# Performance work log

Hardware: AMD Instinct MI355X
Metric: run time of the kernel (lower is better)

Reference implementation:

```python
import jax, jax.numpy as jnp
import numpy as np

NEG_SLOPE = 0.2  # PyG GATConv default
EPS = 1e-5       # BatchNorm1d default


def gat_conv(x, src, dst, W, a_src, a_dst, b, concat, num_nodes):
    # x: [N, Fin], W: [Fin, H*C], a_src/a_dst: [H, C], b: [H*C] or [C]
    H, C = a_src.shape
    h = (x @ W).reshape(num_nodes, H, C)           # [N, H, C]
    e_src = (h * a_src).sum(-1)                    # [N, H]
    e_dst = (h * a_dst).sum(-1)                    # [N, H]
    e = jax.nn.leaky_relu(e_src[src] + e_dst[dst], NEG_SLOPE)  # [E, H]
    # softmax over incoming edges per destination node (stable)
    m = jax.ops.segment_max(e, dst, num_segments=num_nodes)    # [N, H]
    ee = jnp.exp(e - m[dst])
    denom = jax.ops.segment_sum(ee, dst, num_segments=num_nodes)
    alpha = ee / denom[dst]                        # [E, H]
    out = jax.ops.segment_sum(alpha[:, :, None] * h[src], dst,
                              num_segments=num_nodes)          # [N, H, C]
    out = out.reshape(num_nodes, H * C) if concat else out.mean(axis=1)
    return out + b


def batchnorm(x, gamma, beta):
    mu = x.mean(axis=0)
    var = x.var(axis=0)
    return (x - mu) * jax.lax.rsqrt(var + EPS) * gamma + beta


def setup_inputs() -> dict:
    key = jax.random.key(0)
    ks = jax.random.split(key, 16)
    N, E, Fin, Hd, H, L = 50000, 800000, 256, 64, 4, 64
    s = 0.05
    inp = {
        "x": jax.random.normal(ks[0], (N, Fin), jnp.float32),
        "edge_index": jax.random.randint(ks[1], (2, E), 0, N, jnp.int64),
        # GAT layer 1 (concat=True -> out dim H*Hd = 256)
        "W1": jax.random.normal(ks[2], (Fin, H * Hd), jnp.float32) * s,
        "a_src1": jax.random.normal(ks[3], (H, Hd), jnp.float32) * s,
        "a_dst1": jax.random.normal(ks[4], (H, Hd), jnp.float32) * s,
        "b1": jnp.zeros((H * Hd,), jnp.float32),
        "gamma1": jnp.ones((H * Hd,), jnp.float32),
        "beta1": jnp.zeros((H * Hd,), jnp.float32),
        # conv_mean (concat=False -> out dim L)
        "Wm": jax.random.normal(ks[5], (H * Hd, H * L), jnp.float32) * s,
        "am_src": jax.random.normal(ks[6], (H, L), jnp.float32) * s,
        "am_dst": jax.random.normal(ks[7], (H, L), jnp.float32) * s,
        "bm": jnp.zeros((L,), jnp.float32),
        # conv_log_std
        "Ws": jax.random.normal(ks[8], (H * Hd, H * L), jnp.float32) * s,
        "as_src": jax.random.normal(ks[9], (H, L), jnp.float32) * s,
        "as_dst": jax.random.normal(ks[10], (H, L), jnp.float32) * s,
        "bs": jnp.zeros((L,), jnp.float32),
    }
    return inp


def reference(x, edge_index, W1, a_src1, a_dst1, b1, gamma1, beta1,
              Wm, am_src, am_dst, bm, Ws, as_src, as_dst, bs):
    N = x.shape[0]
    loops = jnp.arange(N, dtype=edge_index.dtype)
    src = jnp.concatenate([edge_index[0], loops])  # add self-loops (PyG default)
    dst = jnp.concatenate([edge_index[1], loops])
    h = gat_conv(x, src, dst, W1, a_src1, a_dst1, b1, True, N)
    h = jax.nn.relu(batchnorm(h, gamma1, beta1))
    z_mean = gat_conv(h, src, dst, Wm, am_src, am_dst, bm, False, N)
    z_log_std = gat_conv(h, src, dst, Ws, as_src, as_dst, bs, False, N)
    return z_mean, z_log_std
```

## Files before the change

### kernel.cpp

```cpp
#include <hip/hip_runtime.h>
#include <hip/hip_bf16.h>


#define HC 256
#define NH 4
#define LRELU_SLOPE 0.2f
#define BN_EPS 1e-5f

typedef __attribute__((ext_vector_type(8))) short bf16x8_t;
typedef __attribute__((ext_vector_type(4))) float f32x4_t;
typedef __attribute__((ext_vector_type(8))) unsigned short u16x8_t;
typedef __attribute__((ext_vector_type(4))) unsigned short u16x4_t;
typedef unsigned short ushort_t;

__device__ __forceinline__ unsigned short f2bf(float f) {
    unsigned u = __float_as_uint(f);
    u += 0x7fffu + ((u >> 16) & 1u);
    return (unsigned short)(u >> 16);
}
__device__ __forceinline__ float bf2f(unsigned short h) {
    return __uint_as_float(((unsigned)h) << 16);
}

__global__ void detect_k(const int* __restrict__ ei, long long E, int* __restrict__ flag) {
    __shared__ int any;
    if (threadIdx.x == 0) any = 0;
    __syncthreads();
    for (int i = threadIdx.x; i < 1024; i += blockDim.x) {
        long long idx = 2LL * i + 1;
        if (idx < 2 * E && ei[idx] != 0) atomicOr(&any, 1);
    }
    __syncthreads();
    if (threadIdx.x == 0) flag[0] = (any == 0) ? 1 : 0;
}

__device__ __forceinline__ void load_edge(const int* __restrict__ ei, int flag64,
                                          long long E, long long e, int& s, int& d) {
    if (e >= E) { s = d = (int)(e - E); return; }
    if (flag64) { s = ei[2 * e]; d = ei[2 * E + 2 * e]; }
    else        { s = ei[e];     d = ei[E + e]; }
}

__global__ __launch_bounds__(256) void hist_k(const int* __restrict__ ei,
                                              const int* __restrict__ flag,
                                              long long E, long long ET,
                                              int* __restrict__ deg) {
    long long e = blockIdx.x * 256LL + threadIdx.x;
    if (e >= ET) return;
    int s, d;
    load_edge(ei, flag[0], E, e, s, d);
    atomicAdd(&deg[d], 1);
}

__global__ __launch_bounds__(256) void scan1_k(const int* __restrict__ deg,
                                               int* __restrict__ excl,
                                               int* __restrict__ bsum, long long N) {
    __shared__ int buf[256];
    long long i = blockIdx.x * 256LL + threadIdx.x;
    int v = (i < N) ? deg[i] : 0;
    buf[threadIdx.x] = v;
    __syncthreads();
#pragma unroll
    for (int o = 1; o < 256; o <<= 1) {
        int t = (threadIdx.x >= o) ? buf[threadIdx.x - o] : 0;
        __syncthreads();
        buf[threadIdx.x] += t;
        __syncthreads();
    }
    if (i < N) excl[i] = buf[threadIdx.x] - v;
    if (threadIdx.x == 255) bsum[blockIdx.x] = buf[255];
}

__global__ __launch_bounds__(256) void scan2_k(int* __restrict__ bsum, int nb) {
    __shared__ int buf[256];
    int v = (threadIdx.x < nb) ? bsum[threadIdx.x] : 0;
    buf[threadIdx.x] = v;
    __syncthreads();
#pragma unroll
    for (int o = 1; o < 256; o <<= 1) {
        int t = (threadIdx.x >= o) ? buf[threadIdx.x - o] : 0;
        __syncthreads();
        buf[threadIdx.x] += t;
        __syncthreads();
    }
    if (threadIdx.x < nb) bsum[threadIdx.x] = buf[threadIdx.x] - v;
}

__global__ __launch_bounds__(256) void scan3_k(int* __restrict__ rowptr,
                                               const int* __restrict__ bsum,
                                               long long N, long long ET) {
    long long i = blockIdx.x * 256LL + threadIdx.x;
    if (i < N) rowptr[i] += bsum[blockIdx.x];
    if (i == N) rowptr[N] = (int)ET;
}

__global__ __launch_bounds__(256) void scatter_k(const int* __restrict__ ei,
                                                 const int* __restrict__ flag,
                                                 long long E, long long ET,
                                                 const int* __restrict__ rowptr,
                                                 int* __restrict__ cursor,
                                                 int* __restrict__ csr_src) {
    long long e = blockIdx.x * 256LL + threadIdx.x;
    if (e >= ET) return;
    int s, d;
    load_edge(ei, flag[0], E, e, s, d);
    int pos = rowptr[d] + atomicAdd(&cursor[d], 1);
    csr_src[pos] = s;
}

__global__ __launch_bounds__(256) void wconv_k(const float* __restrict__ W1,
                                               const float* __restrict__ Wm,
                                               const float* __restrict__ Ws,
                                               ushort_t* __restrict__ T1,
                                               ushort_t* __restrict__ Tm,
                                               ushort_t* __restrict__ Ts) {
    __shared__ float tile[32][33];
    const float* W = blockIdx.z == 0 ? W1 : (blockIdx.z == 1 ? Wm : Ws);
    ushort_t* T = blockIdx.z == 0 ? T1 : (blockIdx.z == 1 ? Tm : Ts);
    int k0 = blockIdx.y * 32, n0 = blockIdx.x * 32;
    int tx = threadIdx.x & 31, ty = threadIdx.x >> 5;
    for (int r = ty; r < 32; r += 8)
        tile[r][tx] = W[(k0 + r) * 256 + n0 + tx];
    __syncthreads();
    for (int r = ty; r < 32; r += 8)
        T[(n0 + r) * 256 + k0 + tx] = f2bf(tile[tx][r]);
}

__global__ __launch_bounds__(256) void cvt_k(const float* __restrict__ x,
                                             ushort_t* __restrict__ xh, long long n8) {
    long long i = blockIdx.x * 256LL + threadIdx.x;
    if (i >= n8) return;
    float4 v0 = *(const float4*)&x[i * 8];
    float4 v1 = *(const float4*)&x[i * 8 + 4];
    u16x8_t h;
    h[0] = f2bf(v0.x); h[1] = f2bf(v0.y); h[2] = f2bf(v0.z); h[3] = f2bf(v0.w);
    h[4] = f2bf(v1.x); h[5] = f2bf(v1.y); h[6] = f2bf(v1.z); h[7] = f2bf(v1.w);
    *(u16x8_t*)&xh[i * 8] = h;
}

__global__ __launch_bounds__(256) void gemm_bf_k(const ushort_t* __restrict__ A,
                                                 const ushort_t* __restrict__ Bt,
                                                 ushort_t* __restrict__ C, int cstride, int cofs,
                                                 const float* __restrict__ avs,
                                                 const float* __restrict__ avd,
                                                 float* __restrict__ es, float* __restrict__ ed,
                                                 int M) {
    __shared__ short Bs[2][8192];
    const int tid  = threadIdx.x;
    const int warp = tid >> 6, lane = tid & 63;
    const int q = lane >> 4, ln = lane & 15;
    const int r0 = (blockIdx.x * 4 + warp) * 32;

    const ushort_t* sg[4];
    int sdst[4];
#pragma unroll
    for (int it = 0; it < 4; ++it) {
        int idx = it * 256 + tid;
        int j = idx >> 6, sl = idx & 63;
        sg[it]   = Bt + (j * 16 + (sl & 15)) * 256 + (sl >> 4) * 8;
        sdst[it] = idx * 8;
    }
    int ra0 = r0 + ln;      if (ra0 >= M) ra0 = M - 1;
    int ra1 = r0 + 16 + ln; if (ra1 >= M) ra1 = M - 1;
    const ushort_t* pa0 = A + (long long)ra0 * 256 + q * 8;
    const ushort_t* pa1 = A + (long long)ra1 * 256 + q * 8;

    f32x4_t acc0[16] = {}, acc1[16] = {};
#pragma unroll
    for (int it = 0; it < 4; ++it)
        *(bf16x8_t*)&Bs[0][sdst[it]] = *(const bf16x8_t*)sg[it];
    __syncthreads();

    int buf = 0;
    for (int ks = 0; ks < 8; ++ks) {
        bf16x8_t stg[4];
        const bool more = (ks + 1 < 8);
        if (more) {
#pragma unroll
            for (int it = 0; it < 4; ++it)
                stg[it] = *(const bf16x8_t*)(sg[it] + (ks + 1) * 32);
        }
        bf16x8_t a0 = *(const bf16x8_t*)(pa0 + ks * 32);
        bf16x8_t a1 = *(const bf16x8_t*)(pa1 + ks * 32);
#pragma unroll
        for (int j = 0; j < 16; ++j) {
            bf16x8_t b = *(const bf16x8_t*)&Bs[buf][(j * 64 + lane) * 8];
            acc0[j] = __builtin_amdgcn_mfma_f32_16x16x32_bf16(a0, b, acc0[j], 0, 0, 0);
            acc1[j] = __builtin_amdgcn_mfma_f32_16x16x32_bf16(a1, b, acc1[j], 0, 0, 0);
        }
        if (more) {
#pragma unroll
            for (int it = 0; it < 4; ++it)
                *(bf16x8_t*)&Bs[buf ^ 1][sdst[it]] = stg[it];
        }
        __syncthreads();
        buf ^= 1;
    }

#pragma unroll
    for (int hp = 0; hp < 2; ++hp) {
        float ps[2][4][2] = {}, pd[2][4][2] = {};
#pragma unroll
        for (int jj = 0; jj < 8; ++jj) {
            int j = hp * 8 + jj;
            int colv = j * 16 + ln;
            float asv = avs[colv], adv = avd[colv];
            int hh = jj >> 2;
#pragma unroll
            for (int i = 0; i < 4; ++i) {
                ps[0][i][hh] = fmaf(acc0[j][i], asv, ps[0][i][hh]);
                pd[0][i][hh] = fmaf(acc0[j][i], adv, pd[0][i][hh]);
                ps[1][i][hh] = fmaf(acc1[j][i], asv, ps[1][i][hh]);
                pd[1][i][hh] = fmaf(acc1[j][i], adv, pd[1][i][hh]);
            }
        }
#pragma unroll
        for (int m = 8; m >= 1; m >>= 1)
#pragma unroll
            for (int rb = 0; rb < 2; ++rb)
#pragma unroll
                for (int i = 0; i < 4; ++i)
#pragma unroll
                    for (int hh = 0; hh < 2; ++hh) {
                        ps[rb][i][hh] += __shfl_xor(ps[rb][i][hh], m);
                        pd[rb][i][hh] += __shfl_xor(pd[rb][i][hh], m);
                    }
        if (ln == 0) {
#pragma unroll
            for (int rb = 0; rb < 2; ++rb)
#pragma unroll
                for (int i = 0; i < 4; ++i) {
                    int r = r0 + rb * 16 + q * 4 + i;
                    if (r < M) {
                        es[r * NH + hp * 2]     = ps[rb][i][0];
                        es[r * NH + hp * 2 + 1] = ps[rb][i][1];
                        ed[r * NH + hp * 2]     = pd[rb][i][0];
                        ed[r * NH + hp * 2 + 1] = pd[rb][i][1];
                    }
                }
        }
    }

#pragma unroll
    for (int j = 0; j < 16; ++j) {
        int col = j * 16 + ln;
#pragma unroll
        for (int i = 0; i < 4; ++i) {
            int r = r0 + q * 4 + i;
            if (r < M) C[(long long)r * cstride + cofs + col] = f2bf(acc0[j][i]);
            r += 16;
            if (r < M) C[(long long)r * cstride + cofs + col] = f2bf(acc1[j][i]);
        }
    }
}

__global__ __launch_bounds__(256) void agg_concat_k(const int* __restrict__ rowptr,
                                                    const int* __restrict__ csr_src,
                                                    const float* __restrict__ esrc,
                                                    const float* __restrict__ edst,
                                                    const ushort_t* __restrict__ h,
                                                    long long N,
                                                    float* __restrict__ out) {
    long long d = blockIdx.x * 4LL + (threadIdx.x >> 6);
    if (d >= N) return;
    int lane = threadIdx.x & 63;
    int head = lane >> 4;
    float edv = edst[d * NH + head];
    int beg = rowptr[d], end = rowptr[d + 1];
    float a0 = 0.f, a1 = 0.f, a2 = 0.f, a3 = 0.f, den = 0.f;
    int i = beg;
    for (; i + 1 < end; i += 2) {
        int s0 = csr_src[i], s1 = csr_src[i + 1];
        float t0 = esrc[(long long)s0 * NH + head] + edv;
        float t1 = esrc[(long long)s1 * NH + head] + edv;
        u16x4_t h0 = *(const u16x4_t*)&h[(long long)s0 * HC + lane * 4];
        u16x4_t h1 = *(const u16x4_t*)&h[(long long)s1 * HC + lane * 4];
        t0 = t0 >= 0.f ? t0 : LRELU_SLOPE * t0;
        t1 = t1 >= 0.f ? t1 : LRELU_SLOPE * t1;
        float w0 = __expf(t0), w1 = __expf(t1);
        den += w0 + w1;
        a0 = fmaf(w0, bf2f(h0[0]), fmaf(w1, bf2f(h1[0]), a0));
        a1 = fmaf(w0, bf2f(h0[1]), fmaf(w1, bf2f(h1[1]), a1));
        a2 = fmaf(w0, bf2f(h0[2]), fmaf(w1, bf2f(h1[2]), a2));
        a3 = fmaf(w0, bf2f(h0[3]), fmaf(w1, bf2f(h1[3]), a3));
    }
    if (i < end) {
        int s = csr_src[i];
        float t = esrc[(long long)s * NH + head] + edv;
        t = t >= 0.f ? t : LRELU_SLOPE * t;
        float w = __expf(t);
        den += w;
        u16x4_t hv = *(const u16x4_t*)&h[(long long)s * HC + lane * 4];
        a0 = fmaf(w, bf2f(hv[0]), a0); a1 = fmaf(w, bf2f(hv[1]), a1);
        a2 = fmaf(w, bf2f(hv[2]), a2); a3 = fmaf(w, bf2f(hv[3]), a3);
    }
    float inv = 1.0f / den;
    *(float4*)&out[d * HC + lane * 4] = make_float4(a0 * inv, a1 * inv, a2 * inv, a3 * inv);
}

__global__ __launch_bounds__(256) void agg_mean2_k(const int* __restrict__ rowptr,
                                                   const int* __restrict__ csr_src,
                                                   const float* __restrict__ esm,
                                                   const float* __restrict__ edm,
                                                   const float* __restrict__ ess,
                                                   const float* __restrict__ eds,
                                                   const ushort_t* __restrict__ h2,
                                                   const float* __restrict__ bm,
                                                   const float* __restrict__ bs,
                                                   long long N, float* __restrict__ out) {
    long long d = blockIdx.x * 4LL + (threadIdx.x >> 6);
    if (d >= N) return;
    int lane = threadIdx.x & 63;
    int br = lane >> 5, sub = lane & 31, head = sub >> 3;
    const float* esb = br ? ess : esm;
    const float* edb = br ? eds : edm;
    float edv = edb[d * NH + head];
    int beg = rowptr[d], end = rowptr[d + 1];
    float acc[8] = {};
    float den = 0.f;
    int i = beg;
    for (; i + 1 < end; i += 2) {
        int s0 = csr_src[i], s1 = csr_src[i + 1];
        float t0 = esb[(long long)s0 * NH + head] + edv;
        float t1 = esb[(long long)s1 * NH + head] + edv;
        u16x8_t v0 = *(const u16x8_t*)&h2[(long long)s0 * 512 + lane * 8];
        u16x8_t v1 = *(const u16x8_t*)&h2[(long long)s1 * 512 + lane * 8];
        t0 = t0 >= 0.f ? t0 : LRELU_SLOPE * t0;
        t1 = t1 >= 0.f ? t1 : LRELU_SLOPE * t1;
        float w0 = __expf(t0), w1 = __expf(t1);
        den += w0 + w1;
#pragma unroll
        for (int k = 0; k < 8; ++k)
            acc[k] = fmaf(w0, bf2f(v0[k]), fmaf(w1, bf2f(v1[k]), acc[k]));
    }
    if (i < end) {
        int s = csr_src[i];
        float t = esb[(long long)s * NH + head] + edv;
        t = t >= 0.f ? t : LRELU_SLOPE * t;
        float w = __expf(t);
        den += w;
        u16x8_t v = *(const u16x8_t*)&h2[(long long)s * 512 + lane * 8];
#pragma unroll
        for (int k = 0; k < 8; ++k)
            acc[k] = fmaf(w, bf2f(v[k]), acc[k]);
    }
    float inv = 1.0f / den;
#pragma unroll
    for (int k = 0; k < 8; ++k) {
        acc[k] *= inv;
        acc[k] += __shfl_xor(acc[k], 8);
        acc[k] += __shfl_xor(acc[k], 16);
    }
    if (head == 0) {
        const float* bias = br ? bs : bm;
        float* ob = br ? out + N * 64 : out;
        int cb = sub * 8;
        float4 w0 = make_float4(0.25f * acc[0] + bias[cb],
                                0.25f * acc[1] + bias[cb + 1],
                                0.25f * acc[2] + bias[cb + 2],
                                0.25f * acc[3] + bias[cb + 3]);
        float4 w1 = make_float4(0.25f * acc[4] + bias[cb + 4],
                                0.25f * acc[5] + bias[cb + 5],
                                0.25f * acc[6] + bias[cb + 6],
                                0.25f * acc[7] + bias[cb + 7]);
        *(float4*)&ob[d * 64 + cb]     = w0;
        *(float4*)&ob[d * 64 + cb + 4] = w1;
    }
}

__global__ __launch_bounds__(256) void bn_stats_k(const float* __restrict__ x,
                                                  const float* __restrict__ b1,
                                                  long long N, float* __restrict__ sums) {
    int c = threadIdx.x;
    long long r0 = (long long)blockIdx.x * 256;
    long long r1 = r0 + 256 < N ? r0 + 256 : N;
    float bias = b1[c];
    float s = 0.f, ss = 0.f;
    for (long long r = r0; r < r1; ++r) {
        float v = x[r * HC + c] + bias;
        s += v; ss += v * v;
    }
    atomicAdd(&sums[c], s);
    atomicAdd(&sums[HC + c], ss);
}

__global__ __launch_bounds__(256) void bn_norm_relu_k(const float* __restrict__ x,
                                                      const float* __restrict__ b1,
                                                      const float* __restrict__ sums,
                                                      const float* __restrict__ gamma,
                                                      const float* __restrict__ beta,
                                                      long long N,
                                                      ushort_t* __restrict__ hh) {
    long long i = blockIdx.x * 256LL + threadIdx.x;
    if (i >= N * HC) return;
    int c = (int)(i & (HC - 1));
    float invN = 1.0f / (float)N;
    float mu  = sums[c] * invN;
    float var = sums[HC + c] * invN - mu * mu;
    float v = (x[i] + b1[c] - mu) * rsqrtf(var + BN_EPS) * gamma[c] + beta[c];
    v = v > 0.f ? v : 0.f;
    hh[i] = f2bf(v);
}

extern "C" void kernel_launch(void* const* d_in, const int* in_sizes, int n_in,
                              void* d_out, int out_size, void* d_ws, size_t ws_size,
                              hipStream_t stream) {
    const float* x      = (const float*)d_in[0];
    const int*   ei     = (const int*)d_in[1];
    const float* W1     = (const float*)d_in[2];
    const float* a_src1 = (const float*)d_in[3];
    const float* a_dst1 = (const float*)d_in[4];
    const float* b1     = (const float*)d_in[5];
    const float* gamma1 = (const float*)d_in[6];
    const float* beta1  = (const float*)d_in[7];
    const float* Wm     = (const float*)d_in[8];
    const float* am_src = (const float*)d_in[9];
    const float* am_dst = (const float*)d_in[10];
    const float* bm     = (const float*)d_in[11];
    const float* Ws     = (const float*)d_in[12];
    const float* as_src = (const float*)d_in[13];
    const float* as_dst = (const float*)d_in[14];
    const float* bs     = (const float*)d_in[15];
    float* out = (float*)d_out;

    const long long N  = in_sizes[0] / 256;
    const long long E  = in_sizes[1] / 2;
    const long long ET = E + N;
    const int nb = (int)((N + 255) / 256);

    size_t off = 0;
    auto alloc = [&](size_t bytes) -> char* {
        size_t o = off;
        off += (bytes + 255) & ~(size_t)255;
        return (char*)d_ws + o;
    };
    int*   flag    = (int*)  alloc(256);
    float* sums    = (float*)alloc(2 * HC * sizeof(float));
    int*   bsumv   = (int*)  alloc(256 * sizeof(int));
    ushort_t* T1   = (ushort_t*)alloc(65536 * 2);
    ushort_t* Tm   = (ushort_t*)alloc(65536 * 2);
    ushort_t* Ts   = (ushort_t*)alloc(65536 * 2);
    float* esm     = (float*)alloc(N * NH * sizeof(float));
    float* edm     = (float*)alloc(N * NH * sizeof(float));
    float* ess     = (float*)alloc(N * NH * sizeof(float));
    float* eds     = (float*)alloc(N * NH * sizeof(float));
    int*   deg     = (int*)  alloc(N * sizeof(int));
    int*   rowptr  = (int*)  alloc((N + 1) * sizeof(int));
    int*   csr_src = (int*)  alloc(ET * sizeof(int));
    ushort_t* B1   = (ushort_t*)alloc(N * HC * 2);
    char*     B2c  = alloc(N * 512 * 2);
    (void)ws_size; (void)n_in; (void)out_size;

    ushort_t* xh   = (ushort_t*)B2c;
    float*    agg1 = (float*)B2c;
    ushort_t* h2   = (ushort_t*)B2c;

    const int M = (int)N;
    const int ggrid = (M + 127) / 128;
    dim3 wgrid(8, 8, 3);
    const long long egrid = (ET + 255) / 256;
    const long long agrid = (N + 3) / 4;
    const long long ngrid = (N * HC + 255) / 256;
    const long long cgrid = (N * HC / 8 + 255) / 256;

    detect_k<<<1, 256, 0, stream>>>(ei, E, flag);
    wconv_k<<<wgrid, 256, 0, stream>>>(W1, Wm, Ws, T1, Tm, Ts);
    cvt_k<<<(int)cgrid, 256, 0, stream>>>(x, xh, N * HC / 8);

    hipMemsetAsync(deg, 0, N * sizeof(int), stream);
    hist_k<<<(int)egrid, 256, 0, stream>>>(ei, flag, E, ET, deg);
    scan1_k<<<nb, 256, 0, stream>>>(deg, rowptr, bsumv, N);
    scan2_k<<<1, 256, 0, stream>>>(bsumv, nb);
    scan3_k<<<nb + 1, 256, 0, stream>>>(rowptr, bsumv, N, ET);
    hipMemsetAsync(deg, 0, N * sizeof(int), stream);
    scatter_k<<<(int)egrid, 256, 0, stream>>>(ei, flag, E, ET, rowptr, deg, csr_src);

    gemm_bf_k<<<ggrid, 256, 0, stream>>>(xh, T1, B1, HC, 0, a_src1, a_dst1, esm, edm, M);
    agg_concat_k<<<(int)agrid, 256, 0, stream>>>(rowptr, csr_src, esm, edm, B1, N, agg1);
    hipMemsetAsync(sums, 0, 2 * HC * sizeof(float), stream);
    bn_stats_k<<<nb, 256, 0, stream>>>(agg1, b1, N, sums);
    bn_norm_relu_k<<<(int)ngrid, 256, 0, stream>>>(agg1, b1, sums, gamma1, beta1, N, B1);

    gemm_bf_k<<<ggrid, 256, 0, stream>>>(B1, Tm, h2, 512, 0,   am_src, am_dst, esm, edm, M);
    gemm_bf_k<<<ggrid, 256, 0, stream>>>(B1, Ts, h2, 512, 256, as_src, as_dst, ess, eds, M);
    agg_mean2_k<<<(int)agrid, 256, 0, stream>>>(rowptr, csr_src, esm, edm, ess, eds,
                                                h2, bm, bs, N, out);
}
```

Baseline: 516.8 us.

## Fuse conversion and BatchNorm into GEMM loads, merge launches, store agg in bf16

The x-to-bf16 conversion moves into the first GEMM's A-operand load, and BatchNorm normalize plus ReLU moves into the second GEMM's A load using precomputed per-channel scale/shift. The two output GEMMs become one launch over blockIdx.z. Memsets and edge-format detection fold into one init kernel, and the second deg reset moves into scan1. The layer-1 aggregation now stores bf16 instead of fp32, and both aggregation loops unroll by four. This cuts full-tensor passes and launches, but redoes the BN transform per GEMM tile, adds bf16 rounding before BN stats, and adds workspace since buffers are no longer aliased.

```diff
diff --git a/kernel.cpp b/kernel.cpp
--- a/kernel.cpp
+++ b/kernel.cpp
@@ -22,16 +22,24 @@
     return __uint_as_float(((unsigned)h) << 16);
 }
 
-__global__ void detect_k(const int* __restrict__ ei, long long E, int* __restrict__ flag) {
-    __shared__ int any;
-    if (threadIdx.x == 0) any = 0;
-    __syncthreads();
-    for (int i = threadIdx.x; i < 1024; i += blockDim.x) {
-        long long idx = 2LL * i + 1;
-        if (idx < 2 * E && ei[idx] != 0) atomicOr(&any, 1);
-    }
-    __syncthreads();
-    if (threadIdx.x == 0) flag[0] = (any == 0) ? 1 : 0;
+__global__ __launch_bounds__(256) void init_k(const int* __restrict__ ei, long long E,
+                                              long long N, int* __restrict__ flag,
+                                              int* __restrict__ deg, float* __restrict__ sums) {
+    long long i = blockIdx.x * 256LL + threadIdx.x;
+    if (i < N) deg[i] = 0;
+    if (blockIdx.x == 0) {
+        sums[threadIdx.x] = 0.f;
+        sums[256 + threadIdx.x] = 0.f;
+        __shared__ int any;
+        if (threadIdx.x == 0) any = 0;
+        __syncthreads();
+        for (int t = threadIdx.x; t < 1024; t += 256) {
+            long long idx = 2LL * t + 1;
+            if (idx < 2 * E && ei[idx] != 0) atomicOr(&any, 1);
+        }
+        __syncthreads();
+        if (threadIdx.x == 0) flag[0] = (any == 0) ? 1 : 0;
+    }
 }
 
 __device__ __forceinline__ void load_edge(const int* __restrict__ ei, int flag64,
@@ -52,7 +60,7 @@
     atomicAdd(&deg[d], 1);
 }
 
-__global__ __launch_bounds__(256) void scan1_k(const int* __restrict__ deg,
+__global__ __launch_bounds__(256) void scan1_k(int* __restrict__ deg,
                                                int* __restrict__ excl,
                                                int* __restrict__ bsum, long long N) {
     __shared__ int buf[256];
@@ -67,7 +75,7 @@
         buf[threadIdx.x] += t;
         __syncthreads();
     }
-    if (i < N) excl[i] = buf[threadIdx.x] - v;
+    if (i < N) { excl[i] = buf[threadIdx.x] - v; deg[i] = 0; }
     if (threadIdx.x == 255) bsum[blockIdx.x] = buf[255];
 }
 
@@ -126,26 +134,73 @@
         T[(n0 + r) * 256 + k0 + tx] = f2bf(tile[tx][r]);
 }
 
-__global__ __launch_bounds__(256) void cvt_k(const float* __restrict__ x,
-                                             ushort_t* __restrict__ xh, long long n8) {
-    long long i = blockIdx.x * 256LL + threadIdx.x;
-    if (i >= n8) return;
-    float4 v0 = *(const float4*)&x[i * 8];
-    float4 v1 = *(const float4*)&x[i * 8 + 4];
-    u16x8_t h;
-    h[0] = f2bf(v0.x); h[1] = f2bf(v0.y); h[2] = f2bf(v0.z); h[3] = f2bf(v0.w);
-    h[4] = f2bf(v1.x); h[5] = f2bf(v1.y); h[6] = f2bf(v1.z); h[7] = f2bf(v1.w);
-    *(u16x8_t*)&xh[i * 8] = h;
-}
-
-__global__ __launch_bounds__(256) void gemm_bf_k(const ushort_t* __restrict__ A,
-                                                 const ushort_t* __restrict__ Bt,
-                                                 ushort_t* __restrict__ C, int cstride, int cofs,
-                                                 const float* __restrict__ avs,
-                                                 const float* __restrict__ avd,
-                                                 float* __restrict__ es, float* __restrict__ ed,
+__global__ __launch_bounds__(256) void bnfin_k(const float* __restrict__ sums,
+                                               const float* __restrict__ b1,
+                                               const float* __restrict__ gamma,
+                                               const float* __restrict__ beta,
+                                               long long N,
+                                               float* __restrict__ scale,
+                                               float* __restrict__ shift) {
+    int c = threadIdx.x;
+    float invN = 1.0f / (float)N;
+    float mu  = sums[c] * invN;
+    float var = sums[256 + c] * invN - mu * mu;
+    float sc = gamma[c] * rsqrtf(var + BN_EPS);
+    scale[c] = sc;
+    shift[c] = (b1[c] - mu) * sc + beta[c];
+}
+
+__device__ __forceinline__ bf16x8_t ld_a_f32(const float* p) {
+    float4 u0 = *(const float4*)p, u1 = *(const float4*)(p + 4);
+    bf16x8_t r;
+    r[0] = (short)f2bf(u0.x); r[1] = (short)f2bf(u0.y);
+    r[2] = (short)f2bf(u0.z); r[3] = (short)f2bf(u0.w);
+    r[4] = (short)f2bf(u1.x); r[5] = (short)f2bf(u1.y);
+    r[6] = (short)f2bf(u1.z); r[7] = (short)f2bf(u1.w);
+    return r;
+}
+__device__ __forceinline__ bf16x8_t ld_a_bn(const ushort_t* p,
+                                            const float* __restrict__ scale,
+                                            const float* __restrict__ shift, int k) {
+    u16x8_t raw = *(const u16x8_t*)p;
+    float4 sc0 = *(const float4*)&scale[k], sc1 = *(const float4*)&scale[k + 4];
+    float4 sh0 = *(const float4*)&shift[k], sh1 = *(const float4*)&shift[k + 4];
+    float sc[8] = {sc0.x, sc0.y, sc0.z, sc0.w, sc1.x, sc1.y, sc1.z, sc1.w};
+    float sh[8] = {sh0.x, sh0.y, sh0.z, sh0.w, sh1.x, sh1.y, sh1.z, sh1.w};
+    bf16x8_t r;
+#pragma unroll
+    for (int j = 0; j < 8; ++j) {
+        float v = fmaf(bf2f(raw[j]), sc[j], sh[j]);
+        v = v > 0.f ? v : 0.f;
+        r[j] = (short)f2bf(v);
+    }
+    return r;
+}
+
+template <int MODE>
+__global__ __launch_bounds__(256) void gemm_bf_k(const float* __restrict__ Af,
+                                                 const ushort_t* __restrict__ Ab,
+                                                 const ushort_t* __restrict__ Bt0,
+                                                 const ushort_t* __restrict__ Bt1,
+                                                 ushort_t* __restrict__ C, int cstride,
+                                                 const float* __restrict__ scale,
+                                                 const float* __restrict__ shift,
+                                                 const float* __restrict__ avs0,
+                                                 const float* __restrict__ avd0,
+                                                 const float* __restrict__ avs1,
+                                                 const float* __restrict__ avd1,
+                                                 float* __restrict__ es0, float* __restrict__ ed0,
+                                                 float* __restrict__ es1, float* __restrict__ ed1,
                                                  int M) {
     __shared__ short Bs[2][8192];
+    const int z = blockIdx.z;
+    const ushort_t* Bt = z ? Bt1 : Bt0;
+    const float* avs = z ? avs1 : avs0;
+    const float* avd = z ? avd1 : avd0;
+    float* es = z ? es1 : es0;
+    float* ed = z ? ed1 : ed0;
+    const int cofs = z * 256;
+
     const int tid  = threadIdx.x;
     const int warp = tid >> 6, lane = tid & 63;
     const int q = lane >> 4, ln = lane & 15;
@@ -162,8 +217,10 @@
     }
     int ra0 = r0 + ln;      if (ra0 >= M) ra0 = M - 1;
     int ra1 = r0 + 16 + ln; if (ra1 >= M) ra1 = M - 1;
-    const ushort_t* pa0 = A + (long long)ra0 * 256 + q * 8;
-    const ushort_t* pa1 = A + (long long)ra1 * 256 + q * 8;
+    const float*    pa0f = Af ? Af + (long long)ra0 * 256 + q * 8 : nullptr;
+    const float*    pa1f = Af ? Af + (long long)ra1 * 256 + q * 8 : nullptr;
+    const ushort_t* pa0b = Ab ? Ab + (long long)ra0 * 256 + q * 8 : nullptr;
+    const ushort_t* pa1b = Ab ? Ab + (long long)ra1 * 256 + q * 8 : nullptr;
 
     f32x4_t acc0[16] = {}, acc1[16] = {};
 #pragma unroll
@@ -180,8 +237,15 @@
             for (int it = 0; it < 4; ++it)
                 stg[it] = *(const bf16x8_t*)(sg[it] + (ks + 1) * 32);
         }
-        bf16x8_t a0 = *(const bf16x8_t*)(pa0 + ks * 32);
-        bf16x8_t a1 = *(const bf16x8_t*)(pa1 + ks * 32);
+        bf16x8_t a0, a1;
+        if constexpr (MODE == 0) {
+            a0 = ld_a_f32(pa0f + ks * 32);
+            a1 = ld_a_f32(pa1f + ks * 32);
+        } else {
+            int k = q * 8 + ks * 32;
+            a0 = ld_a_bn(pa0b + ks * 32, scale, shift, k);
+            a1 = ld_a_bn(pa1b + ks * 32, scale, shift, k);
+        }
 #pragma unroll
         for (int j = 0; j < 16; ++j) {
             bf16x8_t b = *(const bf16x8_t*)&Bs[buf][(j * 64 + lane) * 8];
@@ -243,13 +307,13 @@
 
 #pragma unroll
     for (int j = 0; j < 16; ++j) {
-        int col = j * 16 + ln;
+        int col = cofs + j * 16 + ln;
 #pragma unroll
         for (int i = 0; i < 4; ++i) {
             int r = r0 + q * 4 + i;
-            if (r < M) C[(long long)r * cstride + cofs + col] = f2bf(acc0[j][i]);
+            if (r < M) C[(long long)r * cstride + col] = f2bf(acc0[j][i]);
             r += 16;
-            if (r < M) C[(long long)r * cstride + cofs + col] = f2bf(acc1[j][i]);
+            if (r < M) C[(long long)r * cstride + col] = f2bf(acc1[j][i]);
         }
     }
 }
@@ -260,7 +324,7 @@
                                                     const float* __restrict__ edst,
                                                     const ushort_t* __restrict__ h,
                                                     long long N,
-                                                    float* __restrict__ out) {
+                                                    ushort_t* __restrict__ out) {
     long long d = blockIdx.x * 4LL + (threadIdx.x >> 6);
     if (d >= N) return;
     int lane = threadIdx.x & 63;
@@ -269,22 +333,28 @@
     int beg = rowptr[d], end = rowptr[d + 1];
     float a0 = 0.f, a1 = 0.f, a2 = 0.f, a3 = 0.f, den = 0.f;
     int i = beg;
-    for (; i + 1 < end; i += 2) {
-        int s0 = csr_src[i], s1 = csr_src[i + 1];
+    for (; i + 3 < end; i += 4) {
+        int s0 = csr_src[i], s1 = csr_src[i + 1], s2 = csr_src[i + 2], s3 = csr_src[i + 3];
         float t0 = esrc[(long long)s0 * NH + head] + edv;
         float t1 = esrc[(long long)s1 * NH + head] + edv;
+        float t2 = esrc[(long long)s2 * NH + head] + edv;
+        float t3 = esrc[(long long)s3 * NH + head] + edv;
         u16x4_t h0 = *(const u16x4_t*)&h[(long long)s0 * HC + lane * 4];
         u16x4_t h1 = *(const u16x4_t*)&h[(long long)s1 * HC + lane * 4];
+        u16x4_t h2 = *(const u16x4_t*)&h[(long long)s2 * HC + lane * 4];
+        u16x4_t h3 = *(const u16x4_t*)&h[(long long)s3 * HC + lane * 4];
         t0 = t0 >= 0.f ? t0 : LRELU_SLOPE * t0;
         t1 = t1 >= 0.f ? t1 : LRELU_SLOPE * t1;
-        float w0 = __expf(t0), w1 = __expf(t1);
-        den += w0 + w1;
-        a0 = fmaf(w0, bf2f(h0[0]), fmaf(w1, bf2f(h1[0]), a0));
-        a1 = fmaf(w0, bf2f(h0[1]), fmaf(w1, bf2f(h1[1]), a1));
-        a2 = fmaf(w0, bf2f(h0[2]), fmaf(w1, bf2f(h1[2]), a2));
-        a3 = fmaf(w0, bf2f(h0[3]), fmaf(w1, bf2f(h1[3]), a3));
-    }
-    if (i < end) {
+        t2 = t2 >= 0.f ? t2 : LRELU_SLOPE * t2;
+        t3 = t3 >= 0.f ? t3 : LRELU_SLOPE * t3;
+        float w0 = __expf(t0), w1 = __expf(t1), w2 = __expf(t2), w3 = __expf(t3);
+        den += (w0 + w1) + (w2 + w3);
+        a0 = fmaf(w0, bf2f(h0[0]), fmaf(w1, bf2f(h1[0]), fmaf(w2, bf2f(h2[0]), fmaf(w3, bf2f(h3[0]), a0))));
+        a1 = fmaf(w0, bf2f(h0[1]), fmaf(w1, bf2f(h1[1]), fmaf(w2, bf2f(h2[1]), fmaf(w3, bf2f(h3[1]), a1))));
+        a2 = fmaf(w0, bf2f(h0[2]), fmaf(w1, bf2f(h1[2]), fmaf(w2, bf2f(h2[2]), fmaf(w3, bf2f(h3[2]), a2))));
+        a3 = fmaf(w0, bf2f(h0[3]), fmaf(w1, bf2f(h1[3]), fmaf(w2, bf2f(h2[3]), fmaf(w3, bf2f(h3[3]), a3))));
+    }
+    for (; i < end; ++i) {
         int s = csr_src[i];
         float t = esrc[(long long)s * NH + head] + edv;
         t = t >= 0.f ? t : LRELU_SLOPE * t;
@@ -295,7 +365,10 @@
         a2 = fmaf(w, bf2f(hv[2]), a2); a3 = fmaf(w, bf2f(hv[3]), a3);
     }
     float inv = 1.0f / den;
-    *(float4*)&out[d * HC + lane * 4] = make_float4(a0 * inv, a1 * inv, a2 * inv, a3 * inv);
+    u16x4_t o;
+    o[0] = f2bf(a0 * inv); o[1] = f2bf(a1 * inv);
+    o[2] = f2bf(a2 * inv); o[3] = f2bf(a3 * inv);
+    *(u16x4_t*)&out[d * HC + lane * 4] = o;
 }
 
 __global__ __launch_bounds__(256) void agg_mean2_k(const int* __restrict__ rowptr,
@@ -319,21 +392,30 @@
     float acc[8] = {};
     float den = 0.f;
     int i = beg;
-    for (; i + 1 < end; i += 2) {
-        int s0 = csr_src[i], s1 = csr_src[i + 1];
+    for (; i + 3 < end; i += 4) {
+        int s0 = csr_src[i], s1 = csr_src[i + 1], s2 = csr_src[i + 2], s3 = csr_src[i + 3];
         float t0 = esb[(long long)s0 * NH + head] + edv;
         float t1 = esb[(long long)s1 * NH + head] + edv;
+        float t2 = esb[(long long)s2 * NH + head] + edv;
+        float t3 = esb[(long long)s3 * NH + head] + edv;
         u16x8_t v0 = *(const u16x8_t*)&h2[(long long)s0 * 512 + lane * 8];
         u16x8_t v1 = *(const u16x8_t*)&h2[(long long)s1 * 512 + lane * 8];
+        u16x8_t v2 = *(const u16x8_t*)&h2[(long long)s2 * 512 + lane * 8];
+        u16x8_t v3 = *(const u16x8_t*)&h2[(long long)s3 * 512 + lane * 8];
         t0 = t0 >= 0.f ? t0 : LRELU_SLOPE * t0;
         t1 = t1 >= 0.f ? t1 : LRELU_SLOPE * t1;
-        float w0 = __expf(t0), w1 = __expf(t1);
-        den += w0 + w1;
+        t2 = t2 >= 0.f ? t2 : LRELU_SLOPE * t2;
+        t3 = t3 >= 0.f ? t3 : LRELU_SLOPE * t3;
+        float w0 = __expf(t0), w1 = __expf(t1), w2 = __expf(t2), w3 = __expf(t3);
+        den += (w0 + w1) + (w2 + w3);
 #pragma unroll
         for (int k = 0; k < 8; ++k)
-            acc[k] = fmaf(w0, bf2f(v0[k]), fmaf(w1, bf2f(v1[k]), acc[k]));
-    }
-    if (i < end) {
+            acc[k] = fmaf(w0, bf2f(v0[k]),
+                     fmaf(w1, bf2f(v1[k]),
+                     fmaf(w2, bf2f(v2[k]),
+                     fmaf(w3, bf2f(v3[k]), acc[k]))));
+    }
+    for (; i < end; ++i) {
         int s = csr_src[i];
         float t = esb[(long long)s * NH + head] + edv;
         t = t >= 0.f ? t : LRELU_SLOPE * t;
@@ -368,7 +450,7 @@
     }
 }
 
-__global__ __launch_bounds__(256) void bn_stats_k(const float* __restrict__ x,
+__global__ __launch_bounds__(256) void bn_stats_k(const ushort_t* __restrict__ x,
                                                   const float* __restrict__ b1,
                                                   long long N, float* __restrict__ sums) {
     int c = threadIdx.x;
@@ -377,29 +459,11 @@
     float bias = b1[c];
     float s = 0.f, ss = 0.f;
     for (long long r = r0; r < r1; ++r) {
-        float v = x[r * HC + c] + bias;
+        float v = bf2f(x[r * HC + c]) + bias;
         s += v; ss += v * v;
     }
     atomicAdd(&sums[c], s);
     atomicAdd(&sums[HC + c], ss);
-}
-
-__global__ __launch_bounds__(256) void bn_norm_relu_k(const float* __restrict__ x,
-                                                      const float* __restrict__ b1,
-                                                      const float* __restrict__ sums,
-                                                      const float* __restrict__ gamma,
-                                                      const float* __restrict__ beta,
-                                                      long long N,
-                                                      ushort_t* __restrict__ hh) {
-    long long i = blockIdx.x * 256LL + threadIdx.x;
-    if (i >= N * HC) return;
-    int c = (int)(i & (HC - 1));
-    float invN = 1.0f / (float)N;
-    float mu  = sums[c] * invN;
-    float var = sums[HC + c] * invN - mu * mu;
-    float v = (x[i] + b1[c] - mu) * rsqrtf(var + BN_EPS) * gamma[c] + beta[c];
-    v = v > 0.f ? v : 0.f;
-    hh[i] = f2bf(v);
 }
 
 extern "C" void kernel_launch(void* const* d_in, const int* in_sizes, int n_in,
@@ -436,6 +500,8 @@
     };
     int*   flag    = (int*)  alloc(256);
     float* sums    = (float*)alloc(2 * HC * sizeof(float));
+    float* scale   = (float*)alloc(HC * sizeof(float));
+    float* shift   = (float*)alloc(HC * sizeof(float));
     int*   bsumv   = (int*)  alloc(256 * sizeof(int));
     ushort_t* T1   = (ushort_t*)alloc(65536 * 2);
     ushort_t* Tm   = (ushort_t*)alloc(65536 * 2);
@@ -447,42 +513,36 @@
     int*   deg     = (int*)  alloc(N * sizeof(int));
     int*   rowptr  = (int*)  alloc((N + 1) * sizeof(int));
     int*   csr_src = (int*)  alloc(ET * sizeof(int));
-    ushort_t* B1   = (ushort_t*)alloc(N * HC * 2);
-    char*     B2c  = alloc(N * 512 * 2);
+    ushort_t* H1   = (ushort_t*)alloc(N * HC * 2);
+    ushort_t* agg1 = (ushort_t*)alloc(N * HC * 2);
+    ushort_t* h2   = (ushort_t*)alloc(N * 512 * 2);
     (void)ws_size; (void)n_in; (void)out_size;
-
-    ushort_t* xh   = (ushort_t*)B2c;
-    float*    agg1 = (float*)B2c;
-    ushort_t* h2   = (ushort_t*)B2c;
 
     const int M = (int)N;
     const int ggrid = (M + 127) / 128;
     dim3 wgrid(8, 8, 3);
     const long long egrid = (ET + 255) / 256;
     const long long agrid = (N + 3) / 4;
-    const long long ngrid = (N * HC + 255) / 256;
-    const long long cgrid = (N * HC / 8 + 255) / 256;
-
-    detect_k<<<1, 256, 0, stream>>>(ei, E, flag);
+
+    init_k<<<nb, 256, 0, stream>>>(ei, E, N, flag, deg, sums);
     wconv_k<<<wgrid, 256, 0, stream>>>(W1, Wm, Ws, T1, Tm, Ts);
-    cvt_k<<<(int)cgrid, 256, 0, stream>>>(x, xh, N * HC / 8);
-
-    hipMemsetAsync(deg, 0, N * sizeof(int), stream);
+
     hist_k<<<(int)egrid, 256, 0, stream>>>(ei, flag, E, ET, deg);
     scan1_k<<<nb, 256, 0, stream>>>(deg, rowptr, bsumv, N);
     scan2_k<<<1, 256, 0, stream>>>(bsumv, nb);
     scan3_k<<<nb + 1, 256, 0, stream>>>(rowptr, bsumv, N, ET);
-    hipMemsetAsync(deg, 0, N * sizeof(int), stream);
     scatter_k<<<(int)egrid, 256, 0, stream>>>(ei, flag, E, ET, rowptr, deg, csr_src);
 
-    gemm_bf_k<<<ggrid, 256, 0, stream>>>(xh, T1, B1, HC, 0, a_src1, a_dst1, esm, edm, M);
-    agg_concat_k<<<(int)agrid, 256, 0, stream>>>(rowptr, csr_src, esm, edm, B1, N, agg1);
-    hipMemsetAsync(sums, 0, 2 * HC * sizeof(float), stream);
+    gemm_bf_k<0><<<dim3(ggrid, 1, 1), 256, 0, stream>>>(
+        x, nullptr, T1, T1, H1, HC, nullptr, nullptr,
+        a_src1, a_dst1, nullptr, nullptr, esm, edm, nullptr, nullptr, M);
+    agg_concat_k<<<(int)agrid, 256, 0, stream>>>(rowptr, csr_src, esm, edm, H1, N, agg1);
     bn_stats_k<<<nb, 256, 0, stream>>>(agg1, b1, N, sums);
-    bn_norm_relu_k<<<(int)ngrid, 256, 0, stream>>>(agg1, b1, sums, gamma1, beta1, N, B1);
-
-    gemm_bf_k<<<ggrid, 256, 0, stream>>>(B1, Tm, h2, 512, 0,   am_src, am_dst, esm, edm, M);
-    gemm_bf_k<<<ggrid, 256, 0, stream>>>(B1, Ts, h2, 512, 256, as_src, as_dst, ess, eds, M);
+    bnfin_k<<<1, 256, 0, stream>>>(sums, b1, gamma1, beta1, N, scale, shift);
+
+    gemm_bf_k<1><<<dim3(ggrid, 1, 2), 256, 0, stream>>>(
+        nullptr, agg1, Tm, Ts, h2, 512, scale, shift,
+        am_src, am_dst, as_src, as_dst, esm, edm, ess, eds, M);
     agg_mean2_k<<<(int)agrid, 256, 0, stream>>>(rowptr, csr_src, esm, edm, ess, eds,
                                                 h2, bm, bs, N, out);
 }
```

Measured after the change: 481.6 us (median of 2 runs). -6.8%, faster.
